# Optimization experiments

Hardware: AMD Instinct MI355X
Metric: run time of the kernel (lower is better)

Reference implementation:

```python
import jax, jax.numpy as jnp
import numpy as np

K = 3  # kernel_size

def _bn(x, g, b, m, v, eps=1e-5):
    # inference-mode BatchNorm2d over channel axis 1
    sh = (1, -1, 1, 1)
    return (x - m.reshape(sh)) * (g.reshape(sh) / jnp.sqrt(v.reshape(sh) + eps)) + b.reshape(sh)

def setup_inputs() -> dict:
    key = jax.random.key(0)
    ks = jax.random.split(key, 12)
    B, C, H, W, OC = 8, 128, 96, 96, 256
    k2 = K * K
    x = jax.random.normal(ks[0], (B, C, H, W), jnp.float32)
    # get_weight grouped 1x1 conv: [C*9,1,1,1] stored compactly as [C,9]
    w1 = jax.random.normal(ks[1], (C, k2), jnp.float32) * 0.1
    # generate_feature grouped 3x3 conv (groups=C, multiplier 9): OIHW [C*9,1,3,3]
    gf_w = jax.random.normal(ks[2], (C * k2, 1, K, K), jnp.float32) * 0.1
    bn1_g = jax.random.uniform(ks[3], (C * k2,), jnp.float32, 0.5, 1.5)
    bn1_b = jax.random.normal(ks[4], (C * k2,), jnp.float32) * 0.1
    bn1_m = jax.random.normal(ks[5], (C * k2,), jnp.float32) * 0.1
    bn1_v = jax.random.uniform(ks[6], (C * k2,), jnp.float32, 0.5, 1.5)
    conv_w = jax.random.normal(ks[7], (OC, C, K, K), jnp.float32) * (1.0 / np.sqrt(C * k2))
    conv_b = jax.random.normal(ks[8], (OC,), jnp.float32) * 0.1
    bn2_g = jax.random.uniform(ks[9], (OC,), jnp.float32, 0.5, 1.5)
    bn2_b = jax.random.normal(ks[10], (OC,), jnp.float32) * 0.1
    bn2_m = jax.random.normal(ks[11], (OC,), jnp.float32) * 0.1
    bn2_v = jax.random.uniform(jax.random.fold_in(key, 99), (OC,), jnp.float32, 0.5, 1.5)
    return {"x": x, "w1": w1, "gf_w": gf_w, "bn1_g": bn1_g, "bn1_b": bn1_b,
            "bn1_m": bn1_m, "bn1_v": bn1_v, "conv_w": conv_w, "conv_b": conv_b,
            "bn2_g": bn2_g, "bn2_b": bn2_b, "bn2_m": bn2_m, "bn2_v": bn2_v}

def reference(x, w1, gf_w, bn1_g, bn1_b, bn1_m, bn1_v, conv_w, conv_b, bn2_g, bn2_b, bn2_m, bn2_v):
    B, C, H, W = x.shape
    k2 = K * K
    # --- get_weight: AvgPool2d(k=3, pad=1, stride=1, count_include_pad) + grouped 1x1 conv ---
    pooled = jax.lax.reduce_window(x, 0.0, jax.lax.add, (1, 1, K, K), (1, 1, 1, 1),
                                   [(0, 0), (0, 0), (1, 1), (1, 1)]) / float(k2)
    weight = jnp.einsum('bchw,cn->bcnhw', pooled, w1)  # [B,C,9,H,W]
    attn = jax.nn.softmax(weight, axis=2)
    # --- generate_feature: depthwise 3x3 conv (groups=C, mult 9) + BN + ReLU ---
    feat = jax.lax.conv_general_dilated(x, gf_w, (1, 1), [(1, 1), (1, 1)],
                                        dimension_numbers=('NCHW', 'OIHW', 'NCHW'),
                                        feature_group_count=C)
    feat = jax.nn.relu(_bn(feat, bn1_g, bn1_b, bn1_m, bn1_v)).reshape(B, C, k2, H, W)
    # --- attention reweight + space-to-depth rearrange 'b c (n1 n2) h w -> b c (h n1) (w n2)' ---
    wd = (feat * attn).reshape(B, C, K, K, H, W)
    wd = wd.transpose(0, 1, 4, 2, 5, 3).reshape(B, C, H * K, W * K)
    # --- final conv k=3 stride=3 + BN + ReLU ---
    out = jax.lax.conv_general_dilated(wd, conv_w, (K, K), [(0, 0), (0, 0)],
                                       dimension_numbers=('NCHW', 'OIHW', 'NCHW'))
    out = out + conv_b.reshape(1, -1, 1, 1)
    return jax.nn.relu(_bn(out, bn2_g, bn2_b, bn2_m, bn2_v))
```

## Files before the change

### kernel.cpp

```cpp
#include <hip/hip_runtime.h>
#include <hip/hip_bf16.h>


#define CCH  128
#define OCN  256
#define HH   96
#define WWD  96
#define KCH  1152
#define PIMG 9216
#define BNP  64
#define NBLK 144
#define CC   32
#define KC   288
#define VP   296
#define NT   512

using short8  = __attribute__((ext_vector_type(8))) short;
using f32x4   = __attribute__((ext_vector_type(4))) float;
using float4v = __attribute__((ext_vector_type(4))) float;

__device__ __forceinline__ ushort bf16bits(float f) {
    __hip_bfloat16 h = __float2bfloat16(f);
    return *reinterpret_cast<ushort*>(&h);
}

__global__ void prep_kernel(const float* __restrict__ W2, const float* __restrict__ gfw,
                            const float* __restrict__ bn1g, const float* __restrict__ bn1b,
                            const float* __restrict__ bn1m, const float* __restrict__ bn1v,
                            const float* __restrict__ w1,
                            ushort* __restrict__ W2bf, float* __restrict__ gws,
                            float* __restrict__ shiftv, float* __restrict__ w1s) {
    int i = blockIdx.x * 256 + threadIdx.x;
    if (i < OCN * KCH) {
        W2bf[i] = bf16bits(W2[i]);
    } else if (i < OCN * KCH + KCH) {
        const int ch = i - OCN * KCH;
        const float sc = bn1g[ch] * rsqrtf(bn1v[ch] + 1e-5f);
        shiftv[ch] = bn1b[ch] - bn1m[ch] * sc;
        #pragma unroll
        for (int t = 0; t < 9; ++t) gws[ch * 12 + t] = gfw[ch * 9 + t] * sc;
    } else if (i < OCN * KCH + KCH + CCH) {
        const int c = i - OCN * KCH - KCH;
        #pragma unroll
        for (int n = 0; n < 9; ++n) w1s[c * 12 + n] = w1[c * 9 + n] * (1.f / 9.f);
    }
}

template<bool FAST>
__global__ __launch_bounds__(NT, 4) void rfa_mfma2_kernel(
    const float* __restrict__ x,
    const float* __restrict__ w1,   const float* __restrict__ gfw,
    const float* __restrict__ bn1g, const float* __restrict__ bn1b,
    const float* __restrict__ bn1m, const float* __restrict__ bn1v,
    const float* __restrict__ W2f,
    const ushort* __restrict__ W2bf, const float* __restrict__ gws,
    const float* __restrict__ shiftv, const float* __restrict__ w1s,
    const float* __restrict__ cbias,
    const float* __restrict__ bn2g, const float* __restrict__ bn2b,
    const float* __restrict__ bn2m, const float* __restrict__ bn2v,
    float* __restrict__ out)
{
    __shared__ ushort vlds[2][BNP * VP];

    const int tid = threadIdx.x;
    const int b   = blockIdx.x / NBLK;
    const int P0  = (blockIdx.x % NBLK) * BNP;

    const int px  = tid & 63;
    const int p   = P0 + px;
    const int h   = p / WWD;
    const int w   = p - h * WWD;
    const int wid = tid >> 6;
    const int l15 = px & 15;
    const int lhi = px >> 4;

    f32x4 acc[2][4] = {};

    const float* xb = x + (size_t)b * CCH * PIMG;
    const int abase = (wid * 32 + l15) * KCH + lhi * 8;

    for (int ck = 0; ck < 4; ++ck) {
        ushort* vbuf = vlds[ck & 1];

        #pragma unroll 2
        for (int pass = 0; pass < 4; ++pass) {
            const int cl = wid * 4 + pass;
            const int c  = ck * CC + cl;
            const float* xc = xb + (size_t)c * PIMG;

            float nb[9];
            #pragma unroll
            for (int dy = 0; dy < 3; ++dy) {
                const int hy = h + dy - 1;
                const bool hok = (unsigned)hy < (unsigned)HH;
                const float* xr = xc + hy * WWD;
                #pragma unroll
                for (int dx = 0; dx < 3; ++dx) {
                    const int wx = w + dx - 1;
                    const bool ok = hok && ((unsigned)wx < (unsigned)WWD);
                    nb[dy * 3 + dx] = ok ? xr[wx] : 0.f;
                }
            }
            float psum = 0.f;
            #pragma unroll
            for (int t = 0; t < 9; ++t) psum += nb[t];

            float at[9];
            float ss = 0.f;
            if constexpr (FAST) {
                const float* w1r = w1s + c * 12;
                #pragma unroll
                for (int n = 0; n < 9; ++n) { at[n] = __expf(psum * w1r[n]); ss += at[n]; }
            } else {
                const float pooled = psum * (1.f / 9.f);
                const float* w1r = w1 + c * 9;
                #pragma unroll
                for (int n = 0; n < 9; ++n) { at[n] = __expf(pooled * w1r[n]); ss += at[n]; }
            }
            const float rs = 1.f / ss;

            const int ch0 = c * 9;
            ushort* vp = vbuf + px * VP + cl * 9;
            #pragma unroll
            for (int n = 0; n < 9; ++n) {
                const int ch = ch0 + n;
                float f;
                if constexpr (FAST) {
                    const float* gr = gws + ch * 12;
                    f = shiftv[ch];
                    #pragma unroll
                    for (int t = 0; t < 9; ++t) f = fmaf(nb[t], gr[t], f);
                } else {
                    const float* gr = gfw + ch * 9;
                    float cv = 0.f;
                    #pragma unroll
                    for (int t = 0; t < 9; ++t) cv = fmaf(nb[t], gr[t], cv);
                    const float sc = bn1g[ch] * rsqrtf(bn1v[ch] + 1e-5f);
                    f = (cv - bn1m[ch]) * sc + bn1b[ch];
                }
                f = fmaxf(f, 0.f) * (at[n] * rs);
                vp[n] = bf16bits(f);
            }
        }
        __syncthreads();

        const int k0 = ck * KC;
        #pragma unroll 3
        for (int kk = 0; kk < 9; ++kk) {
            short8 afr[2], bfr[4];
            #pragma unroll
            for (int mi = 0; mi < 2; ++mi) {
                const int ai = abase + mi * 16 * KCH + k0 + kk * 32;
                if constexpr (FAST) {
                    afr[mi] = *reinterpret_cast<const short8*>(W2bf + ai);
                } else {
                    const float4v f0 = *reinterpret_cast<const float4v*>(W2f + ai);
                    const float4v f1 = *reinterpret_cast<const float4v*>(W2f + ai + 4);
                    short8 a;
                    a[0] = (short)bf16bits(f0[0]); a[1] = (short)bf16bits(f0[1]);
                    a[2] = (short)bf16bits(f0[2]); a[3] = (short)bf16bits(f0[3]);
                    a[4] = (short)bf16bits(f1[0]); a[5] = (short)bf16bits(f1[1]);
                    a[6] = (short)bf16bits(f1[2]); a[7] = (short)bf16bits(f1[3]);
                    afr[mi] = a;
                }
            }
            #pragma unroll
            for (int ni = 0; ni < 4; ++ni) {
                const ushort* bp = vbuf + (ni * 16 + l15) * VP + kk * 32 + lhi * 8;
                bfr[ni] = *reinterpret_cast<const short8*>(bp);
            }
            #pragma unroll
            for (int mi = 0; mi < 2; ++mi)
                #pragma unroll
                for (int ni = 0; ni < 4; ++ni)
                    acc[mi][ni] = __builtin_amdgcn_mfma_f32_16x16x32_bf16(
                        afr[mi], bfr[ni], acc[mi][ni], 0, 0, 0);
        }
    }

    #pragma unroll
    for (int mi = 0; mi < 2; ++mi) {
        #pragma unroll
        for (int r = 0; r < 4; ++r) {
            const int oc = wid * 32 + mi * 16 + lhi * 4 + r;
            const float s2 = bn2g[oc] * rsqrtf(bn2v[oc] + 1e-5f);
            const float t2 = (cbias[oc] - bn2m[oc]) * s2 + bn2b[oc];
            float* op = out + ((size_t)(b * OCN + oc)) * PIMG + P0;
            #pragma unroll
            for (int ni = 0; ni < 4; ++ni)
                op[ni * 16 + l15] = fmaxf(fmaf(acc[mi][ni][r], s2, t2), 0.f);
        }
    }
}

extern "C" void kernel_launch(void* const* d_in, const int* in_sizes, int n_in,
                              void* d_out, int out_size, void* d_ws, size_t ws_size,
                              hipStream_t stream) {
    const float* xx   = (const float*)d_in[0];
    const float* w1   = (const float*)d_in[1];
    const float* gfw  = (const float*)d_in[2];
    const float* bn1g = (const float*)d_in[3];
    const float* bn1b = (const float*)d_in[4];
    const float* bn1m = (const float*)d_in[5];
    const float* bn1v = (const float*)d_in[6];
    const float* W2   = (const float*)d_in[7];
    const float* cb   = (const float*)d_in[8];
    const float* bn2g = (const float*)d_in[9];
    const float* bn2b = (const float*)d_in[10];
    const float* bn2m = (const float*)d_in[11];
    const float* bn2v = (const float*)d_in[12];
    float* o = (float*)d_out;

    const size_t off_gws   = (size_t)OCN * KCH * sizeof(ushort);
    const size_t off_shift = off_gws + (size_t)KCH * 12 * sizeof(float);
    const size_t off_w1s   = off_shift + (size_t)KCH * sizeof(float);
    const size_t ws_need   = off_w1s + (size_t)CCH * 12 * sizeof(float);

    dim3 grid(8 * NBLK);
    dim3 blk(NT);

    if (ws_size >= ws_need) {
        ushort* W2bf  = (ushort*)d_ws;
        float*  gws   = (float*)((char*)d_ws + off_gws);
        float*  shf   = (float*)((char*)d_ws + off_shift);
        float*  w1s   = (float*)((char*)d_ws + off_w1s);
        const int ptot = OCN * KCH + KCH + CCH;
        prep_kernel<<<(ptot + 255) / 256, 256, 0, stream>>>(
            W2, gfw, bn1g, bn1b, bn1m, bn1v, w1, W2bf, gws, shf, w1s);
        rfa_mfma2_kernel<true><<<grid, blk, 0, stream>>>(
            xx, w1, gfw, bn1g, bn1b, bn1m, bn1v, W2, W2bf, gws, shf, w1s,
            cb, bn2g, bn2b, bn2m, bn2v, o);
    } else {
        rfa_mfma2_kernel<false><<<grid, blk, 0, stream>>>(
            xx, w1, gfw, bn1g, bn1b, bn1m, bn1v, W2, nullptr, nullptr, nullptr, nullptr,
            cb, bn2g, bn2b, bn2m, bn2v, o);
    }
}
```

Baseline: 245.6 us.

## Prefetch next channel's neighbourhood, use clamped branchless loads and packed FMA

The neighbourhood gather now uses precomputed clamped row and column offsets with a multiplicative validity mask in place of per-element branches. The next channel's 3x3 window is software-prefetched into registers while the current channel is processed, and the pass loop is fully unrolled. The depthwise conv uses packed two-wide FMAs, the softmax normaliser uses a hardware reciprocal, and the wave id is made scalar via readfirstlane. The goal is to hide global-load latency in the feature-generation phase and cut VALU work, at the cost of higher register pressure under the 4-blocks-per-CU launch bound.

Measured after the change: 210.4 us. 1.17x faster.

```diff
diff --git a/kernel.cpp b/kernel.cpp
--- a/kernel.cpp
+++ b/kernel.cpp
@@ -17,12 +17,14 @@
 
 using short8  = __attribute__((ext_vector_type(8))) short;
 using f32x4   = __attribute__((ext_vector_type(4))) float;
-using float4v = __attribute__((ext_vector_type(4))) float;
+using f32x2   = __attribute__((ext_vector_type(2))) float;
 
 __device__ __forceinline__ ushort bf16bits(float f) {
     __hip_bfloat16 h = __float2bfloat16(f);
     return *reinterpret_cast<ushort*>(&h);
 }
+
+struct NB { f32x2 p[4]; float s; };
 
 __global__ void prep_kernel(const float* __restrict__ W2, const float* __restrict__ gfw,
                             const float* __restrict__ bn1g, const float* __restrict__ bn1b,
@@ -46,8 +48,21 @@
     }
 }
 
+__device__ __forceinline__ NB load_nb(const float* __restrict__ xc,
+                                      const int hro0, const int hro1, const int hro2,
+                                      const int wx0, const int wx1, const int wx2) {
+    NB r;
+    float v0 = xc[hro0 + wx0], v1 = xc[hro0 + wx1], v2 = xc[hro0 + wx2];
+    float v3 = xc[hro1 + wx0], v4 = xc[hro1 + wx1], v5 = xc[hro1 + wx2];
+    float v6 = xc[hro2 + wx0], v7 = xc[hro2 + wx1], v8 = xc[hro2 + wx2];
+    r.p[0] = f32x2{v0, v1}; r.p[1] = f32x2{v2, v3};
+    r.p[2] = f32x2{v4, v5}; r.p[3] = f32x2{v6, v7};
+    r.s = v8;
+    return r;
+}
+
 template<bool FAST>
-__global__ __launch_bounds__(NT, 4) void rfa_mfma2_kernel(
+__global__ __launch_bounds__(NT, 4) void rfa_mfma3_kernel(
     const float* __restrict__ x,
     const float* __restrict__ w1,   const float* __restrict__ gfw,
     const float* __restrict__ bn1g, const float* __restrict__ bn1b,
@@ -70,43 +85,62 @@
     const int p   = P0 + px;
     const int h   = p / WWD;
     const int w   = p - h * WWD;
-    const int wid = tid >> 6;
+    const int wid = __builtin_amdgcn_readfirstlane(tid >> 6);
     const int l15 = px & 15;
     const int lhi = px >> 4;
 
+    int hro[3], wxc[3];
+    f32x2 okp[4];
+    float ok8;
+    {
+        float okr[3], okc[3];
+        #pragma unroll
+        for (int d = 0; d < 3; ++d) {
+            int hy = h + d - 1;
+            okr[d] = ((unsigned)hy < (unsigned)HH) ? 1.f : 0.f;
+            hro[d] = ((hy < 0) ? 0 : (hy > 95 ? 95 : hy)) * WWD;
+            int wx = w + d - 1;
+            okc[d] = ((unsigned)wx < (unsigned)WWD) ? 1.f : 0.f;
+            wxc[d] = (wx < 0) ? 0 : (wx > 95 ? 95 : wx);
+        }
+        float o[9];
+        #pragma unroll
+        for (int dy = 0; dy < 3; ++dy)
+            #pragma unroll
+            for (int dx = 0; dx < 3; ++dx) o[dy*3+dx] = okr[dy] * okc[dx];
+        okp[0] = f32x2{o[0], o[1]}; okp[1] = f32x2{o[2], o[3]};
+        okp[2] = f32x2{o[4], o[5]}; okp[3] = f32x2{o[6], o[7]};
+        ok8 = o[8];
+    }
+
     f32x4 acc[2][4] = {};
-
     const float* xb = x + (size_t)b * CCH * PIMG;
     const int abase = (wid * 32 + l15) * KCH + lhi * 8;
 
+    auto chan = [&](int q) { return (q >> 2) * CC + wid * 4 + (q & 3); };
+
+    NB nb = load_nb(xb + (size_t)chan(0) * PIMG, hro[0], hro[1], hro[2], wxc[0], wxc[1], wxc[2]);
+
     for (int ck = 0; ck < 4; ++ck) {
         ushort* vbuf = vlds[ck & 1];
 
-        #pragma unroll 2
+        #pragma unroll
         for (int pass = 0; pass < 4; ++pass) {
+            const int q  = ck * 4 + pass;
+            const int qn = (q + 1 > 15) ? 15 : q + 1;
+            NB nbn = load_nb(xb + (size_t)chan(qn) * PIMG,
+                             hro[0], hro[1], hro[2], wxc[0], wxc[1], wxc[2]);
+
+            const int c  = chan(q);
             const int cl = wid * 4 + pass;
-            const int c  = ck * CC + cl;
-            const float* xc = xb + (size_t)c * PIMG;
-
-            float nb[9];
-            #pragma unroll
-            for (int dy = 0; dy < 3; ++dy) {
-                const int hy = h + dy - 1;
-                const bool hok = (unsigned)hy < (unsigned)HH;
-                const float* xr = xc + hy * WWD;
-                #pragma unroll
-                for (int dx = 0; dx < 3; ++dx) {
-                    const int wx = w + dx - 1;
-                    const bool ok = hok && ((unsigned)wx < (unsigned)WWD);
-                    nb[dy * 3 + dx] = ok ? xr[wx] : 0.f;
-                }
-            }
-            float psum = 0.f;
-            #pragma unroll
-            for (int t = 0; t < 9; ++t) psum += nb[t];
-
-            float at[9];
-            float ss = 0.f;
+            f32x2 e[4];
+            #pragma unroll
+            for (int i = 0; i < 4; ++i) e[i] = nb.p[i] * okp[i];
+            const float e8 = nb.s * ok8;
+            f32x2 ps2 = (e[0] + e[1]) + (e[2] + e[3]);
+            const float psum = ps2[0] + ps2[1] + e8;
+
+            float at[9], ss = 0.f;
             if constexpr (FAST) {
                 const float* w1r = w1s + c * 12;
                 #pragma unroll
@@ -117,30 +151,35 @@
                 #pragma unroll
                 for (int n = 0; n < 9; ++n) { at[n] = __expf(pooled * w1r[n]); ss += at[n]; }
             }
-            const float rs = 1.f / ss;
-
-            const int ch0 = c * 9;
+            const float rs = __builtin_amdgcn_rcpf(ss);
+
             ushort* vp = vbuf + px * VP + cl * 9;
             #pragma unroll
             for (int n = 0; n < 9; ++n) {
-                const int ch = ch0 + n;
+                const int ch = c * 9 + n;
                 float f;
                 if constexpr (FAST) {
-                    const float* gr = gws + ch * 12;
-                    f = shiftv[ch];
+                    const f32x2* gp = reinterpret_cast<const f32x2*>(gws + ch * 12);
+                    f32x2 f2 = f32x2{shiftv[ch], 0.f};
                     #pragma unroll
-                    for (int t = 0; t < 9; ++t) f = fmaf(nb[t], gr[t], f);
+                    for (int t = 0; t < 4; ++t) f2 = __builtin_elementwise_fma(e[t], gp[t], f2);
+                    f = f2[0] + f2[1];
+                    f = fmaf(e8, gws[ch * 12 + 8], f);
                 } else {
                     const float* gr = gfw + ch * 9;
                     float cv = 0.f;
-                    #pragma unroll
-                    for (int t = 0; t < 9; ++t) cv = fmaf(nb[t], gr[t], cv);
+                    cv = fmaf(e[0][0], gr[0], cv); cv = fmaf(e[0][1], gr[1], cv);
+                    cv = fmaf(e[1][0], gr[2], cv); cv = fmaf(e[1][1], gr[3], cv);
+                    cv = fmaf(e[2][0], gr[4], cv); cv = fmaf(e[2][1], gr[5], cv);
+                    cv = fmaf(e[3][0], gr[6], cv); cv = fmaf(e[3][1], gr[7], cv);
+                    cv = fmaf(e8, gr[8], cv);
                     const float sc = bn1g[ch] * rsqrtf(bn1v[ch] + 1e-5f);
                     f = (cv - bn1m[ch]) * sc + bn1b[ch];
                 }
                 f = fmaxf(f, 0.f) * (at[n] * rs);
                 vp[n] = bf16bits(f);
             }
+            nb = nbn;
         }
         __syncthreads();
 
@@ -154,8 +193,8 @@
                 if constexpr (FAST) {
                     afr[mi] = *reinterpret_cast<const short8*>(W2bf + ai);
                 } else {
-                    const float4v f0 = *reinterpret_cast<const float4v*>(W2f + ai);
-                    const float4v f1 = *reinterpret_cast<const float4v*>(W2f + ai + 4);
+                    const f32x4 f0 = *reinterpret_cast<const f32x4*>(W2f + ai);
+                    const f32x4 f1 = *reinterpret_cast<const f32x4*>(W2f + ai + 4);
                     short8 a;
                     a[0] = (short)bf16bits(f0[0]); a[1] = (short)bf16bits(f0[1]);
                     a[2] = (short)bf16bits(f0[2]); a[3] = (short)bf16bits(f0[3]);
@@ -220,18 +259,18 @@
     dim3 blk(NT);
 
     if (ws_size >= ws_need) {
-        ushort* W2bf  = (ushort*)d_ws;
-        float*  gws   = (float*)((char*)d_ws + off_gws);
-        float*  shf   = (float*)((char*)d_ws + off_shift);
-        float*  w1s   = (float*)((char*)d_ws + off_w1s);
+        ushort* W2bf = (ushort*)d_ws;
+        float*  gwsp = (float*)((char*)d_ws + off_gws);
+        float*  shf  = (float*)((char*)d_ws + off_shift);
+        float*  w1sp = (float*)((char*)d_ws + off_w1s);
         const int ptot = OCN * KCH + KCH + CCH;
         prep_kernel<<<(ptot + 255) / 256, 256, 0, stream>>>(
-            W2, gfw, bn1g, bn1b, bn1m, bn1v, w1, W2bf, gws, shf, w1s);
-        rfa_mfma2_kernel<true><<<grid, blk, 0, stream>>>(
-            xx, w1, gfw, bn1g, bn1b, bn1m, bn1v, W2, W2bf, gws, shf, w1s,
+            W2, gfw, bn1g, bn1b, bn1m, bn1v, w1, W2bf, gwsp, shf, w1sp);
+        rfa_mfma3_kernel<true><<<grid, blk, 0, stream>>>(
+            xx, w1, gfw, bn1g, bn1b, bn1m, bn1v, W2, W2bf, gwsp, shf, w1sp,
             cb, bn2g, bn2b, bn2m, bn2v, o);
     } else {
-        rfa_mfma2_kernel<false><<<grid, blk, 0, stream>>>(
+        rfa_mfma3_kernel<false><<<grid, blk, 0, stream>>>(
             xx, w1, gfw, bn1g, bn1b, bn1m, bn1v, W2, nullptr, nullptr, nullptr, nullptr,
             cb, bn2g, bn2b, bn2m, bn2v, o);
     }
```
